# Kernel tuning notes

Measured on AMD Instinct MI355X. Metric: run time of the kernel, lower is better.

Reference implementation:

```python
import jax, jax.numpy as jnp
import numpy as np

M, H, F, T, IT, NUM_SEM = 256, 256, 256, 4, 2, 50
NEG = jnp.float32(-1e30)


def _lin(k, fi, fo):
    kw, kb = jax.random.split(k)
    s = 1.0 / np.sqrt(fi)
    W = jax.random.uniform(kw, (fi, fo), minval=-s, maxval=s, dtype=jnp.float32)
    b = jax.random.uniform(kb, (fo,), minval=-s, maxval=s, dtype=jnp.float32)
    return W, b


def setup_inputs() -> dict:
    key = jax.random.key(0)
    ks = jax.random.split(key, 16)
    parent_feature = jax.random.normal(ks[0], (1, F), dtype=jnp.float32)
    gt_children_code = jax.random.normal(ks[1], (1, 16), dtype=jnp.float32)
    gt_num_code = jax.random.normal(ks[2], (1, 10), dtype=jnp.float32)
    W_parent, b_parent = _lin(ks[3], F + 26, H * M)
    W_exists, b_exists = _lin(ks[4], H, 1)
    W_sem, b_sem = _lin(ks[5], H, NUM_SEM)
    W_el, b_el = _lin(ks[6], 2 * H, H)          # mlp_edge_latent
    s = 1.0 / np.sqrt(H)
    W_ee = jax.random.uniform(ks[7], (T, H), minval=-s, maxval=s, dtype=jnp.float32)  # stacked mlp_edge_exists
    b_ee = jax.random.uniform(ks[8], (T,), minval=-s, maxval=s, dtype=jnp.float32)
    s2 = 1.0 / np.sqrt(3 * H + T)
    W_ne = jax.random.uniform(ks[9], (IT, 3 * H + T, H), minval=-s2, maxval=s2, dtype=jnp.float32)  # node_edge_op
    b_ne = jax.random.uniform(ks[10], (IT, H), minval=-s2, maxval=s2, dtype=jnp.float32)
    W_child, b_child = _lin(ks[11], H * (IT + 1), H)
    W_child2, b_child2 = _lin(ks[12], H, F)
    return dict(parent_feature=parent_feature, gt_children_code=gt_children_code,
                gt_num_code=gt_num_code, W_parent=W_parent, b_parent=b_parent,
                W_exists=W_exists, b_exists=b_exists, W_sem=W_sem, b_sem=b_sem,
                W_el=W_el, b_el=b_el, W_ee=W_ee, b_ee=b_ee, W_ne=W_ne, b_ne=b_ne,
                W_child=W_child, b_child=b_child, W_child2=W_child2, b_child2=b_child2)


def reference(parent_feature, gt_children_code, gt_num_code, W_parent, b_parent,
              W_exists, b_exists, W_sem, b_sem, W_el, b_el, W_ee, b_ee,
              W_ne, b_ne, W_child, b_child, W_child2, b_child2):
    x = jnp.concatenate([parent_feature, gt_children_code, gt_num_code], axis=1)  # [1, F+26]
    child = jax.nn.relu(x @ W_parent + b_parent).reshape(1, M, H)
    exists_logits = child @ W_exists + b_exists                   # [1, M, 1]
    cf = child[0]                                                 # [M, H]
    # edge latents: relu(Linear(cat(cf_i, cf_j))) without materializing [M,M,2H]
    a = cf @ W_el[:H]
    b2 = cf @ W_el[H:]
    el = jax.nn.relu(a[:, None, :] + b2[None, :, :] + b_el)       # [M, M, H]
    ee = jnp.einsum('mnh,th->mnt', el, W_ee) + b_ee               # [M, M, T]
    # fixed edge set: candidate edges where type-logit>0 and both endpoints exist
    node_ok = exists_logits[0, :, 0] > 0                          # [M]
    mask = (ee > 0) & node_ok[:, None, None] & node_ok[None, :, None]  # [M, M, T]
    has_edges = mask.any()
    iter_feats = [cf]
    for i in range(IT):
        W = W_ne[i]
        Ws, Wd, We, Wt = W[:H], W[H:2 * H], W[2 * H:3 * H], W[3 * H:]
        pre = (cf @ Ws)[:, None, :] + (cf @ Wd)[None, :, :] \
              + jnp.einsum('mnh,hk->mnk', el, We) + b_ne[i]       # [M, M, H]
        # one-hot edge-type logit contribution: etl[e,t]=ee[i,j,t] only at the edge's type
        feats = jax.nn.relu(pre[:, :, None, :] + jnp.einsum('mnt,th->mnth', ee, Wt))  # [M,M,T,H]
        # scatter_max over source node i with zero-initialized output
        new = jnp.max(jnp.where(mask[..., None], feats, NEG), axis=(1, 2))  # [M, H]
        new = jnp.maximum(new, 0.0)
        cf = jnp.where(has_edges, new, cf)
        iter_feats.append(cf)
    cfc = jnp.concatenate(iter_feats, axis=1)                     # [M, H*(IT+1)]
    ch = jax.nn.relu(cfc @ W_child + b_child)                     # [M, H]
    child_sem_logits = (ch @ W_sem + b_sem)[None]                 # [1, M, NUM_SEM]
    child_feats = jax.nn.relu(ch @ W_child2 + b_child2)[None]     # [1, M, F]
    return child_feats, child_sem_logits, exists_logits, ee[None]
```

## Files before the change

kernel.cpp:

```cpp
#include <hip/hip_runtime.h>
#include <hip/hip_bf16.h>
#include <stdint.h>

#define NEGV -1e30f

typedef __attribute__((ext_vector_type(8))) __bf16 bf16x8;
typedef __attribute__((ext_vector_type(4))) float f32x4;

__device__ __forceinline__ uint16_t f2bfu(float f){
  __hip_bfloat16 h = __float2bfloat16(f);
  return *reinterpret_cast<const uint16_t*>(&h);
}

__device__ __forceinline__ void dev_transpose(
  const float* __restrict__ in, __hip_bfloat16* __restrict__ out,
  int K, int N, int ktiles, int b, int tid, float* t)
{
  int kt = b % ktiles, nt = b / ktiles;
  int k0 = kt*64, n0 = nt*64;
  int c = tid & 63, rg = tid >> 6;
  #pragma unroll
  for (int rr = 0; rr < 16; ++rr){
    int row = rg + rr*4;
    t[row*65 + c] = in[(k0+row)*N + n0 + c];
  }
  __syncthreads();
  #pragma unroll
  for (int rr = 0; rr < 16; ++rr){
    int row = rg + rr*4;
    out[(n0+row)*K + k0 + c] = __float2bfloat16(t[c*65 + row]);
  }
}

__global__ __launch_bounds__(256) void k_front(
    const float* __restrict__ pf, const float* __restrict__ gc,
    const float* __restrict__ gn, const float* __restrict__ Wp,
    const float* __restrict__ Wne, const float* __restrict__ Wch,
    const float* __restrict__ Wc2, const float* __restrict__ Wsem,
    float* __restrict__ pchild, __hip_bfloat16* __restrict__ WeT,
    __hip_bfloat16* __restrict__ WchT, __hip_bfloat16* __restrict__ Wc2T,
    __hip_bfloat16* __restrict__ WsemT)
{
  __shared__ float sh[64*65];
  int bid = blockIdx.x, tid = threadIdx.x;
  if (bid < 512){
    int jb = bid & 63, ks = bid >> 6;
    int i0 = ks*36, i1 = (i0+36 < 282) ? i0+36 : 282;
    if (tid < i1-i0){
      int i = i0 + tid;
      sh[tid] = (i < 256) ? pf[i] : ((i < 272) ? gc[i-256] : gn[i-272]);
    }
    __syncthreads();
    int j0 = jb*1024 + tid*4;
    f32x4 acc = {0,0,0,0};
    #pragma unroll 6
    for (int i = i0; i < i1; ++i){
      f32x4 w = *reinterpret_cast<const f32x4*>(Wp + i*65536 + j0);
      float x = sh[i-i0];
      acc[0] = fmaf(x, w[0], acc[0]);
      acc[1] = fmaf(x, w[1], acc[1]);
      acc[2] = fmaf(x, w[2], acc[2]);
      acc[3] = fmaf(x, w[3], acc[3]);
    }
    *reinterpret_cast<f32x4*>(pchild + ks*65536 + j0) = acc;
  } else if (bid < 544){
    int b = bid - 512; int it = b >> 4;
    dev_transpose(Wne + it*197632 + 512*256, WeT + it*65536, 256, 256, 4, b & 15, tid, sh);
  } else if (bid < 592){
    dev_transpose(Wch, WchT, 768, 256, 12, bid - 544, tid, sh);
  } else if (bid < 608){
    dev_transpose(Wc2, Wc2T, 256, 256, 4, bid - 592, tid, sh);
  } else {
    int b = bid - 608;
    int j = b*4 + (tid>>6), c = tid & 63;
    float v = (c < 50) ? Wsem[j*50+c] : 0.f;
    WsemT[c*256 + j] = __float2bfloat16(v);
  }
}

__global__ __launch_bounds__(256) void k_child_reduce_exists(
  const float* __restrict__ pchild, const float* __restrict__ bp,
  const float* __restrict__ Wex, const float* __restrict__ bex,
  float* __restrict__ cf, __hip_bfloat16* __restrict__ cfcb,
  float* __restrict__ exout, int* __restrict__ ok, int* __restrict__ flag)
{
  __shared__ float red[256];
  int m = blockIdx.x, tid = threadIdx.x;
  int j = m*256 + tid;
  float s = bp[j];
  #pragma unroll
  for (int ks = 0; ks < 8; ++ks) s += pchild[ks*65536 + j];
  s = fmaxf(s, 0.f);
  cf[j] = s;
  cfcb[m*768 + tid] = __float2bfloat16(s);
  red[tid] = s * Wex[tid];
  __syncthreads();
  for (int st = 128; st > 0; st >>= 1){ if (tid < st) red[tid] += red[tid+st]; __syncthreads(); }
  if (tid == 0){
    float logit = red[0] + bex[0];
    exout[m] = logit;
    ok[m] = logit > 0.f ? 1 : 0;
    if (m == 0) *flag = 0;
  }
}

__global__ __launch_bounds__(256) void k_ab(
  const float* __restrict__ cf, const float* __restrict__ Wel,
  float* __restrict__ a, float* __restrict__ b2)
{
  __shared__ float cfs[2][256];
  int bid = blockIdx.x; int sel = bid >> 7; int m0 = (bid & 127)*2; int tid = threadIdx.x;
  cfs[0][tid] = cf[m0*256 + tid];
  cfs[1][tid] = cf[(m0+1)*256 + tid];
  __syncthreads();
  const float* W = Wel + sel*65536;
  float acc0 = 0.f, acc1 = 0.f;
  #pragma unroll 8
  for (int j = 0; j < 256; ++j){
    float w = W[j*256+tid];
    acc0 = fmaf(cfs[0][j], w, acc0);
    acc1 = fmaf(cfs[1][j], w, acc1);
  }
  float* dst = sel ? b2 : a;
  dst[m0*256+tid] = acc0;
  dst[(m0+1)*256+tid] = acc1;
}

__global__ __launch_bounds__(256) void k_ee(
  const float* __restrict__ a, const float* __restrict__ b2,
  const float* __restrict__ bel, const float* __restrict__ Wee,
  const float* __restrict__ bee, const int* __restrict__ ok,
  float* __restrict__ eeout, float* __restrict__ eemask, int* __restrict__ flag)
{
  __shared__ float acs[256];
  __shared__ float wee[1024];
  int bid = blockIdx.x; int m = bid >> 2, nt = bid & 3;
  int tid = threadIdx.x;
  acs[tid] = a[m*256+tid] + bel[tid];
  #pragma unroll
  for (int p = 0; p < 4; ++p) wee[p*256+tid] = Wee[p*256+tid];
  __syncthreads();
  int w = tid>>6, l = tid&63, l15 = l&15, lg = l>>4;
  int n = nt*64 + w*16 + l15;
  const float* br = b2 + (size_t)n*256;
  float e[4] = {0.f,0.f,0.f,0.f};
  #pragma unroll
  for (int kk = 0; kk < 8; ++kk){
    int h0 = kk*32 + lg*8;
    f32x4 bb0 = *reinterpret_cast<const f32x4*>(br + h0);
    f32x4 bb1 = *reinterpret_cast<const f32x4*>(br + h0 + 4);
    f32x4 aa0 = *reinterpret_cast<const f32x4*>(acs + h0);
    f32x4 aa1 = *reinterpret_cast<const f32x4*>(acs + h0 + 4);
    float el[8];
    #pragma unroll
    for (int j = 0; j < 4; ++j){
      el[j]   = fmaxf(aa0[j]+bb0[j], 0.f);
      el[j+4] = fmaxf(aa1[j]+bb1[j], 0.f);
    }
    #pragma unroll
    for (int t = 0; t < 4; ++t){
      f32x4 w0 = *reinterpret_cast<const f32x4*>(&wee[t*256+h0]);
      f32x4 w1 = *reinterpret_cast<const f32x4*>(&wee[t*256+h0+4]);
      e[t] += el[0]*w0[0] + el[1]*w0[1] + el[2]*w0[2] + el[3]*w0[3]
            + el[4]*w1[0] + el[5]*w1[1] + el[6]*w1[2] + el[7]*w1[3];
    }
  }
  #pragma unroll
  for (int t = 0; t < 4; ++t){
    float v = e[t];
    v += __shfl_xor(v, 16);
    v += __shfl_xor(v, 32);
    e[t] = v + bee[t];
  }
  bool valid = false;
  if (lg == 0){
    int okmn = ok[m] & ok[n];
    f32x4 eo, em;
    #pragma unroll
    for (int t = 0; t < 4; ++t){
      eo[t] = e[t];
      em[t] = (okmn && e[t] > 0.f) ? e[t] : NEGV;
      valid = valid || (em[t] > -1e29f);
    }
    int idx = (m*256+n)*4;
    *reinterpret_cast<f32x4*>(eeout + idx) = eo;
    *reinterpret_cast<f32x4*>(eemask + idx) = em;
  }
  if (__any(valid) && l == 0) atomicOr(flag, 1);
}

__global__ __launch_bounds__(256) void k_sd(
  const float* __restrict__ cf, const float* __restrict__ Wne,
  const float* __restrict__ bne, float* __restrict__ sp, float* __restrict__ d, int it)
{
  __shared__ float cfs[2][256];
  int bid = blockIdx.x; int sel = bid >> 7; int m0 = (bid & 127)*2; int tid = threadIdx.x;
  cfs[0][tid] = cf[m0*256 + tid];
  cfs[1][tid] = cf[(m0+1)*256 + tid];
  __syncthreads();
  const float* W = Wne + it*197632 + sel*65536;
  float bias = sel ? 0.f : bne[it*256+tid];
  float acc0 = bias, acc1 = bias;
  #pragma unroll 8
  for (int j = 0; j < 256; ++j){
    float w = W[j*256+tid];
    acc0 = fmaf(cfs[0][j], w, acc0);
    acc1 = fmaf(cfs[1][j], w, acc1);
  }
  float* dst = sel ? d : sp;
  dst[m0*256+tid] = acc0;
  dst[(m0+1)*256+tid] = acc1;
}

__global__ __launch_bounds__(256,2) void k_fused_v3(
  const float* __restrict__ a, const float* __restrict__ bel,
  const float* __restrict__ b2, const __hip_bfloat16* __restrict__ wet,
  const float* __restrict__ sp, const float* __restrict__ dmat,
  const float* __restrict__ eemask, const float* __restrict__ Wne_it,
  float* __restrict__ cf, __hip_bfloat16* __restrict__ cfcb,
  const int* __restrict__ flag, int it)
{
  __shared__ __attribute__((aligned(16))) char weS[32768];
  __shared__ __attribute__((aligned(16))) char elS[32768];
  __shared__ float acs[256];
  __shared__ float red[4][64];
  int bid = blockIdx.x; int m = bid >> 2, kc = bid & 3;
  int tid = threadIdx.x;
  acs[tid] = a[m*256+tid] + bel[tid];
  const char* wsrc = reinterpret_cast<const char*>(wet + kc*16384);
  #pragma unroll
  for (int p = 0; p < 8; ++p){
    int i = p*256 + tid;
    int row = i >> 5, colb = (i & 31) << 4;
    int byte = (row << 9) | colb;
    *reinterpret_cast<bf16x8*>(weS + (byte ^ ((row & 7) << 4))) =
      *reinterpret_cast<const bf16x8*>(wsrc + byte);
  }
  __syncthreads();

  int w = tid >> 6, l = tid & 63, l15 = l & 15, lg = l >> 4;
  float spv[4], wtv[4][4];
  #pragma unroll
  for (int kt = 0; kt < 4; ++kt){
    int kcol = kc*64 + kt*16 + l15;
    spv[kt] = sp[m*256+kcol];
    #pragma unroll
    for (int t = 0; t < 4; ++t) wtv[t][kt] = Wne_it[(768+t)*256 + kcol];
  }
  int rowb[4], rowx[4];
  #pragma unroll
  for (int kt = 0; kt < 4; ++kt){
    int row = kt*16 + l15;
    rowb[kt] = row << 9;
    rowx[kt] = (row & 7) << 4;
  }
  int arow = w*16 + l15;
  int abase = (arow << 9) ^ ((arow & 7) << 4);
  float runmax[4] = {NEGV, NEGV, NEGV, NEGV};

  for (int c = 0; c < 4; ++c){
    #pragma unroll
    for (int p = 0; p < 16; ++p){
      int idx = p*256 + tid;
      int row = idx >> 6;
      int h4 = (idx & 63) << 2;
      f32x4 bv = *reinterpret_cast<const f32x4*>(b2 + (size_t)(c*64+row)*256 + h4);
      f32x4 av = *reinterpret_cast<const f32x4*>(acs + h4);
      union { uint16_t u[4]; uint64_t d; } pk;
      #pragma unroll
      for (int j = 0; j < 4; ++j) pk.u[j] = f2bfu(fmaxf(av[j]+bv[j], 0.f));
      int byte = (row << 9) | (h4 << 1);
      *reinterpret_cast<uint64_t*>(elS + (byte ^ ((row & 7) << 4))) = pk.d;
    }
    __syncthreads();

    int nb = c*64 + w*16;
    f32x4 me[4];
    float dv[4][4];
    #pragma unroll
    for (int r = 0; r < 4; ++r){
      int n = nb + lg*4 + r;
      me[r] = *reinterpret_cast<const f32x4*>(eemask + (m*256+n)*4);
      const float* dr = dmat + n*256 + kc*64;
      #pragma unroll
      for (int kt = 0; kt < 4; ++kt) dv[r][kt] = dr[kt*16 + l15];
    }
    bf16x8 Af[8];
    #pragma unroll
    for (int kk = 0; kk < 8; ++kk)
      Af[kk] = *reinterpret_cast<const bf16x8*>(elS + (((arow << 9) | (kk*64 + lg*16)) ^ ((arow & 7) << 4)));

    f32x4 acc0 = {0,0,0,0}, acc1 = {0,0,0,0}, acc2 = {0,0,0,0}, acc3 = {0,0,0,0};
    #pragma unroll
    for (int kk = 0; kk < 8; ++kk){
      int cc = kk*64 + lg*16;
      bf16x8 B0 = *reinterpret_cast<const bf16x8*>(weS + ((rowb[0] + cc) ^ rowx[0]));
      bf16x8 B1 = *reinterpret_cast<const bf16x8*>(weS + ((rowb[1] + cc) ^ rowx[1]));
      bf16x8 B2 = *reinterpret_cast<const bf16x8*>(weS + ((rowb[2] + cc) ^ rowx[2]));
      bf16x8 B3 = *reinterpret_cast<const bf16x8*>(weS + ((rowb[3] + cc) ^ rowx[3]));
      acc0 = __builtin_amdgcn_mfma_f32_16x16x32_bf16(Af[kk], B0, acc0, 0, 0, 0);
      acc1 = __builtin_amdgcn_mfma_f32_16x16x32_bf16(Af[kk], B1, acc1, 0, 0, 0);
      acc2 = __builtin_amdgcn_mfma_f32_16x16x32_bf16(Af[kk], B2, acc2, 0, 0, 0);
      acc3 = __builtin_amdgcn_mfma_f32_16x16x32_bf16(Af[kk], B3, acc3, 0, 0, 0);
    }
    #pragma unroll
    for (int r = 0; r < 4; ++r){
      float Ed0 = acc0[r] + dv[r][0] + spv[0];
      float Ed1 = acc1[r] + dv[r][1] + spv[1];
      float Ed2 = acc2[r] + dv[r][2] + spv[2];
      float Ed3 = acc3[r] + dv[r][3] + spv[3];
      #pragma unroll
      for (int t = 0; t < 4; ++t){
        if (me[r][t] > -1e29f){
          runmax[0] = fmaxf(runmax[0], fmaf(me[r][t], wtv[t][0], Ed0));
          runmax[1] = fmaxf(runmax[1], fmaf(me[r][t], wtv[t][1], Ed1));
          runmax[2] = fmaxf(runmax[2], fmaf(me[r][t], wtv[t][2], Ed2));
          runmax[3] = fmaxf(runmax[3], fmaf(me[r][t], wtv[t][3], Ed3));
        }
      }
    }
    __syncthreads();
  }
  #pragma unroll
  for (int kt = 0; kt < 4; ++kt){
    float v = runmax[kt];
    v = fmaxf(v, __shfl_xor(v, 16));
    v = fmaxf(v, __shfl_xor(v, 32));
    if (l < 16) red[w][kt*16 + l] = v;
  }
  __syncthreads();
  if (tid < 64){
    float v = fmaxf(fmaxf(red[0][tid], red[1][tid]), fmaxf(red[2][tid], red[3][tid]));
    float nv = fmaxf(v, 0.f);
    int kcol = kc*64 + tid;
    float outv = (*flag) ? nv : cf[m*256+kcol];
    cf[m*256+kcol] = outv;
    cfcb[m*768 + 256*(it+1) + kcol] = __float2bfloat16(outv);
  }
}

__global__ __launch_bounds__(256) void k_final_mfma(
  const __hip_bfloat16* __restrict__ cfcb, const __hip_bfloat16* __restrict__ WchT,
  const float* __restrict__ bch, const __hip_bfloat16* __restrict__ Wc2T,
  const float* __restrict__ bc2, const __hip_bfloat16* __restrict__ WsemT,
  const float* __restrict__ bsem, float* __restrict__ feats_out,
  float* __restrict__ sem_out)
{
  __shared__ char chs[8192];
  int tid = threadIdx.x; int w = tid>>6, l = tid&63, l15 = l&15, lg = l>>4;
  int m0 = blockIdx.x*16;

  f32x4 acc[4] = {{0,0,0,0},{0,0,0,0},{0,0,0,0},{0,0,0,0}};
  const __hip_bfloat16* Aptr = cfcb + (m0 + l15)*768;
  #pragma unroll 2
  for (int ks = 0; ks < 24; ++ks){
    int k0 = ks*32 + lg*8;
    bf16x8 Af = *reinterpret_cast<const bf16x8*>(Aptr + k0);
    #pragma unroll
    for (int nt = 0; nt < 4; ++nt){
      int col = w*64 + nt*16 + l15;
      bf16x8 Bf = *reinterpret_cast<const bf16x8*>(WchT + col*768 + k0);
      acc[nt] = __builtin_amdgcn_mfma_f32_16x16x32_bf16(Af, Bf, acc[nt], 0, 0, 0);
    }
  }
  #pragma unroll
  for (int nt = 0; nt < 4; ++nt){
    int col = w*64 + nt*16 + l15;
    float bias = bch[col];
    #pragma unroll
    for (int r = 0; r < 4; ++r){
      int row = lg*4 + r;
      float v = fmaxf(acc[nt][r] + bias, 0.f);
      int byte = ((row*256 + col)*2) ^ ((row&7)<<4);
      *reinterpret_cast<__hip_bfloat16*>(chs + byte) = __float2bfloat16(v);
    }
  }
  __syncthreads();

  f32x4 accf[4] = {{0,0,0,0},{0,0,0,0},{0,0,0,0},{0,0,0,0}};
  f32x4 accs = {0,0,0,0};
  int cols_sem = w*16 + l15;
  #pragma unroll 2
  for (int ks = 0; ks < 8; ++ks){
    int k0 = ks*32 + lg*8;
    int byteA = (l15*512 + k0*2) ^ ((l15&7)<<4);
    bf16x8 Af = *reinterpret_cast<const bf16x8*>(chs + byteA);
    #pragma unroll
    for (int nt = 0; nt < 4; ++nt){
      int col = w*64 + nt*16 + l15;
      bf16x8 Bf = *reinterpret_cast<const bf16x8*>(Wc2T + col*256 + k0);
      accf[nt] = __builtin_amdgcn_mfma_f32_16x16x32_bf16(Af, Bf, accf[nt], 0, 0, 0);
    }
    bf16x8 Bs = *reinterpret_cast<const bf16x8*>(WsemT + cols_sem*256 + k0);
    accs = __builtin_amdgcn_mfma_f32_16x16x32_bf16(Af, Bs, accs, 0, 0, 0);
  }
  #pragma unroll
  for (int nt = 0; nt < 4; ++nt){
    int col = w*64 + nt*16 + l15;
    float bias = bc2[col];
    #pragma unroll
    for (int r = 0; r < 4; ++r){
      int row = m0 + lg*4 + r;
      feats_out[row*256 + col] = fmaxf(accf[nt][r] + bias, 0.f);
    }
  }
  if (cols_sem < 50){
    float bias = bsem[cols_sem];
    #pragma unroll
    for (int r = 0; r < 4; ++r){
      int row = m0 + lg*4 + r;
      sem_out[row*50 + cols_sem] = accs[r] + bias;
    }
  }
}

extern "C" void kernel_launch(void* const* d_in, const int* in_sizes, int n_in,
                              void* d_out, int out_size, void* d_ws, size_t ws_size,
                              hipStream_t stream)
{
  const float* pf  = (const float*)d_in[0];
  const float* gc  = (const float*)d_in[1];
  const float* gn  = (const float*)d_in[2];
  const float* Wp  = (const float*)d_in[3];
  const float* bp  = (const float*)d_in[4];
  const float* Wex = (const float*)d_in[5];
  const float* bex = (const float*)d_in[6];
  const float* Wsem= (const float*)d_in[7];
  const float* bsem= (const float*)d_in[8];
  const float* Wel = (const float*)d_in[9];
  const float* bel = (const float*)d_in[10];
  const float* Wee = (const float*)d_in[11];
  const float* bee = (const float*)d_in[12];
  const float* Wne = (const float*)d_in[13];
  const float* bne = (const float*)d_in[14];
  const float* Wch = (const float*)d_in[15];
  const float* bch = (const float*)d_in[16];
  const float* Wc2 = (const float*)d_in[17];
  const float* bc2 = (const float*)d_in[18];

  float* out = (float*)d_out;
  float* feats_out = out;
  float* sem_out   = out + 65536;
  float* ex_out    = out + 78336;
  float* ee_out    = out + 78592;

  char* ws = (char*)d_ws;
  float* cf    = (float*)(ws);
  float* a_    = (float*)(ws + ( 256u<<10));
  float* b2_   = (float*)(ws + ( 512u<<10));
  float* sp_   = (float*)(ws + (1024u<<10));
  float* dmat  = (float*)(ws + (1280u<<10));
  float* eem   = (float*)(ws + (1536u<<10));
  __hip_bfloat16* WeT   = (__hip_bfloat16*)(ws + (2560u<<10));
  __hip_bfloat16* cfcb  = (__hip_bfloat16*)(ws + (2816u<<10));
  __hip_bfloat16* WchT  = (__hip_bfloat16*)(ws + (3200u<<10));
  __hip_bfloat16* Wc2T  = (__hip_bfloat16*)(ws + (3584u<<10));
  __hip_bfloat16* WsemT = (__hip_bfloat16*)(ws + (3712u<<10));
  int* ok   = (int*)(ws + (3744u<<10));
  int* flag = ok + 256;
  float* pchild = (float*)(ws + (3776u<<10));

  k_front<<<672,256,0,stream>>>(pf,gc,gn,Wp,Wne,Wch,Wc2,Wsem,
                                pchild,WeT,WchT,Wc2T,WsemT);
  k_child_reduce_exists<<<256,256,0,stream>>>(pchild,bp,Wex,bex,cf,cfcb,ex_out,ok,flag);
  k_ab<<<256,256,0,stream>>>(cf,Wel,a_,b2_);
  k_ee<<<1024,256,0,stream>>>(a_,b2_,bel,Wee,bee,ok,ee_out,eem,flag);
  for (int it = 0; it < 2; ++it){
    k_sd<<<256,256,0,stream>>>(cf,Wne,bne,sp_,dmat,it);
    k_fused_v3<<<1024,256,0,stream>>>(a_,bel,b2_,WeT + it*65536,sp_,dmat,eem,
                                      Wne + it*197632,cf,cfcb,flag,it);
  }
  k_final_mfma<<<16,256,0,stream>>>(cfcb,WchT,bch,Wc2T,bc2,WsemT,bsem,feats_out,sem_out);
}
```

Baseline: 176.1 us.

## Split edge-exists computation into transpose, split-H partial, and combine kernels

Replaces the single edge-exists kernel with three kernels. The first transposes b2 so that each thread reads coalesced columns. The second computes partial edge logits over half of H per block, one thread per destination node. The third sums the two partials, adds the bias, applies the mask and sets the flag. The aim is cleaner coalesced loads and no cross-lane shuffle reductions, at the cost of two extra launches and a round trip of the partial buffer through global memory.

```diff
diff --git a/kernel.cpp b/kernel.cpp
--- a/kernel.cpp
+++ b/kernel.cpp
@@ -126,67 +126,83 @@
   dst[(m0+1)*256+tid] = acc1;
 }
 
-__global__ __launch_bounds__(256) void k_ee(
-  const float* __restrict__ a, const float* __restrict__ b2,
+__global__ __launch_bounds__(256) void k_b2t(
+  const float* __restrict__ b2, float* __restrict__ b2T)
+{
+  __shared__ float t[64][65];
+  int bt = blockIdx.x;
+  int n0 = (bt & 3)*64, h0 = (bt >> 2)*64;
+  int tid = threadIdx.x; int c = tid & 63, rg = tid >> 6;
+  #pragma unroll
+  for (int rr = 0; rr < 16; ++rr){
+    int row = rg + rr*4;
+    t[row][c] = b2[(size_t)(n0+row)*256 + h0 + c];
+  }
+  __syncthreads();
+  #pragma unroll
+  for (int rr = 0; rr < 16; ++rr){
+    int row = rg + rr*4;
+    b2T[(size_t)(h0+row)*256 + n0 + c] = t[c][row];
+  }
+}
+
+__global__ __launch_bounds__(256) void k_ee_part(
+  const float* __restrict__ a, const float* __restrict__ b2T,
   const float* __restrict__ bel, const float* __restrict__ Wee,
-  const float* __restrict__ bee, const int* __restrict__ ok,
-  float* __restrict__ eeout, float* __restrict__ eemask, int* __restrict__ flag)
-{
-  __shared__ float acs[256];
-  __shared__ float wee[1024];
-  int bid = blockIdx.x; int m = bid >> 2, nt = bid & 3;
+  float* __restrict__ pee)
+{
+  __shared__ float wee[4][128];
+  __shared__ float ac[128];
+  int bid = blockIdx.x; int m = bid & 255; int hs = bid >> 8;
   int tid = threadIdx.x;
-  acs[tid] = a[m*256+tid] + bel[tid];
-  #pragma unroll
-  for (int p = 0; p < 4; ++p) wee[p*256+tid] = Wee[p*256+tid];
-  __syncthreads();
-  int w = tid>>6, l = tid&63, l15 = l&15, lg = l>>4;
-  int n = nt*64 + w*16 + l15;
-  const float* br = b2 + (size_t)n*256;
-  float e[4] = {0.f,0.f,0.f,0.f};
-  #pragma unroll
-  for (int kk = 0; kk < 8; ++kk){
-    int h0 = kk*32 + lg*8;
-    f32x4 bb0 = *reinterpret_cast<const f32x4*>(br + h0);
-    f32x4 bb1 = *reinterpret_cast<const f32x4*>(br + h0 + 4);
-    f32x4 aa0 = *reinterpret_cast<const f32x4*>(acs + h0);
-    f32x4 aa1 = *reinterpret_cast<const f32x4*>(acs + h0 + 4);
-    float el[8];
-    #pragma unroll
-    for (int j = 0; j < 4; ++j){
-      el[j]   = fmaxf(aa0[j]+bb0[j], 0.f);
-      el[j+4] = fmaxf(aa1[j]+bb1[j], 0.f);
-    }
-    #pragma unroll
-    for (int t = 0; t < 4; ++t){
-      f32x4 w0 = *reinterpret_cast<const f32x4*>(&wee[t*256+h0]);
-      f32x4 w1 = *reinterpret_cast<const f32x4*>(&wee[t*256+h0+4]);
-      e[t] += el[0]*w0[0] + el[1]*w0[1] + el[2]*w0[2] + el[3]*w0[3]
-            + el[4]*w1[0] + el[5]*w1[1] + el[6]*w1[2] + el[7]*w1[3];
-    }
-  }
-  #pragma unroll
-  for (int t = 0; t < 4; ++t){
-    float v = e[t];
-    v += __shfl_xor(v, 16);
-    v += __shfl_xor(v, 32);
-    e[t] = v + bee[t];
-  }
-  bool valid = false;
-  if (lg == 0){
-    int okmn = ok[m] & ok[n];
-    f32x4 eo, em;
-    #pragma unroll
-    for (int t = 0; t < 4; ++t){
-      eo[t] = e[t];
-      em[t] = (okmn && e[t] > 0.f) ? e[t] : NEGV;
-      valid = valid || (em[t] > -1e29f);
-    }
-    int idx = (m*256+n)*4;
-    *reinterpret_cast<f32x4*>(eeout + idx) = eo;
-    *reinterpret_cast<f32x4*>(eemask + idx) = em;
-  }
-  if (__any(valid) && l == 0) atomicOr(flag, 1);
+  int h0 = hs*128;
+  if (tid < 128){
+    ac[tid] = a[m*256 + h0 + tid] + bel[h0 + tid];
+    wee[0][tid] = Wee[      h0 + tid];
+    wee[1][tid] = Wee[256 + h0 + tid];
+  } else {
+    int t = tid - 128;
+    wee[2][t] = Wee[512 + h0 + t];
+    wee[3][t] = Wee[768 + h0 + t];
+  }
+  __syncthreads();
+  int n = tid;
+  float e0 = 0.f, e1 = 0.f, e2 = 0.f, e3 = 0.f;
+  #pragma unroll 8
+  for (int h = 0; h < 128; ++h){
+    float el = fmaxf(ac[h] + b2T[(h0+h)*256 + n], 0.f);
+    e0 = fmaf(el, wee[0][h], e0);
+    e1 = fmaf(el, wee[1][h], e1);
+    e2 = fmaf(el, wee[2][h], e2);
+    e3 = fmaf(el, wee[3][h], e3);
+  }
+  f32x4 p; p[0]=e0; p[1]=e1; p[2]=e2; p[3]=e3;
+  *reinterpret_cast<f32x4*>(pee + ((hs*256+m)*256 + n)*4) = p;
+}
+
+__global__ __launch_bounds__(256) void k_ee_combine(
+  const float* __restrict__ pee, const float* __restrict__ bee,
+  const int* __restrict__ ok, float* __restrict__ eemask,
+  float* __restrict__ eeout, int* __restrict__ flag)
+{
+  int m = blockIdx.x, n = threadIdx.x;
+  f32x4 p0 = *reinterpret_cast<const f32x4*>(pee + ((0*256+m)*256 + n)*4);
+  f32x4 p1 = *reinterpret_cast<const f32x4*>(pee + ((1*256+m)*256 + n)*4);
+  float e0 = bee[0] + p0[0] + p1[0];
+  float e1 = bee[1] + p0[1] + p1[1];
+  float e2 = bee[2] + p0[2] + p1[2];
+  float e3 = bee[3] + p0[3] + p1[3];
+  int idx = (m*256+n)*4;
+  f32x4 eo; eo[0]=e0; eo[1]=e1; eo[2]=e2; eo[3]=e3;
+  *reinterpret_cast<f32x4*>(eeout + idx) = eo;
+  int okmn = ok[m] & ok[n];
+  f32x4 em;
+  em[0] = (okmn && e0 > 0.f) ? e0 : NEGV;
+  em[1] = (okmn && e1 > 0.f) ? e1 : NEGV;
+  em[2] = (okmn && e2 > 0.f) ? e2 : NEGV;
+  em[3] = (okmn && e3 > 0.f) ? e3 : NEGV;
+  *reinterpret_cast<f32x4*>(eemask + idx) = em;
+  if (em[0] > -1e29f || em[1] > -1e29f || em[2] > -1e29f || em[3] > -1e29f) atomicOr(flag, 1);
 }
 
 __global__ __launch_bounds__(256) void k_sd(
@@ -255,7 +271,6 @@
     rowx[kt] = (row & 7) << 4;
   }
   int arow = w*16 + l15;
-  int abase = (arow << 9) ^ ((arow & 7) << 4);
   float runmax[4] = {NEGV, NEGV, NEGV, NEGV};
 
   for (int c = 0; c < 4; ++c){
@@ -448,6 +463,7 @@
   float* cf    = (float*)(ws);
   float* a_    = (float*)(ws + ( 256u<<10));
   float* b2_   = (float*)(ws + ( 512u<<10));
+  float* b2T   = (float*)(ws + ( 768u<<10));
   float* sp_   = (float*)(ws + (1024u<<10));
   float* dmat  = (float*)(ws + (1280u<<10));
   float* eem   = (float*)(ws + (1536u<<10));
@@ -459,12 +475,15 @@
   int* ok   = (int*)(ws + (3744u<<10));
   int* flag = ok + 256;
   float* pchild = (float*)(ws + (3776u<<10));
+  float* pee    = pchild;
 
   k_front<<<672,256,0,stream>>>(pf,gc,gn,Wp,Wne,Wch,Wc2,Wsem,
                                 pchild,WeT,WchT,Wc2T,WsemT);
   k_child_reduce_exists<<<256,256,0,stream>>>(pchild,bp,Wex,bex,cf,cfcb,ex_out,ok,flag);
   k_ab<<<256,256,0,stream>>>(cf,Wel,a_,b2_);
-  k_ee<<<1024,256,0,stream>>>(a_,b2_,bel,Wee,bee,ok,ee_out,eem,flag);
+  k_b2t<<<16,256,0,stream>>>(b2_,b2T);
+  k_ee_part<<<512,256,0,stream>>>(a_,b2T,bel,Wee,pee);
+  k_ee_combine<<<256,256,0,stream>>>(pee,bee,ok,eem,ee_out,flag);
   for (int it = 0; it < 2; ++it){
     k_sd<<<256,256,0,stream>>>(cf,Wne,bne,sp_,dmat,it);
     k_fused_v3<<<1024,256,0,stream>>>(a_,bel,b2_,WeT + it*65536,sp_,dmat,eem,
```

Result: faster. 153.8 us (-12.7%).
